# Kernel optimization log

Measured on AMD Instinct MI355X. Metric: run time of the kernel, lower is better.

The kernel has to match this reference:

```python
import jax, jax.numpy as jnp
import numpy as np

B, S, D, H = 2, 2048, 768, 12
E = D // H  # d_head = 64


def setup_inputs() -> dict:
    key = jax.random.key(0)
    ks = jax.random.split(key, 10)
    scale = 1.0 / np.sqrt(D)
    x = jax.random.normal(ks[0], (B, S, D), dtype=jnp.float32)
    # Additive mask, laid out [H*B, S, S] as the torch forward slices per head.
    attn_mask = jnp.zeros((H * B, S, S), dtype=jnp.float32)
    # Per-head projections (math form: q = x @ Wq[h] + bq[h])
    Wq = jax.random.normal(ks[1], (H, D, E), dtype=jnp.float32) * scale
    bq = jax.random.normal(ks[2], (H, E), dtype=jnp.float32) * 0.01
    Wk = jax.random.normal(ks[3], (H, D, E), dtype=jnp.float32) * scale
    bk = jax.random.normal(ks[4], (H, E), dtype=jnp.float32) * 0.01
    Wv = jax.random.normal(ks[5], (H, D, E), dtype=jnp.float32) * scale
    bv = jax.random.normal(ks[6], (H, E), dtype=jnp.float32) * 0.01
    Wo = jax.random.normal(ks[7], (D, D), dtype=jnp.float32) * scale
    bo = jax.random.normal(ks[8], (D,), dtype=jnp.float32) * 0.01
    return {"x": x, "attn_mask": attn_mask, "Wq": Wq, "bq": bq,
            "Wk": Wk, "bk": bk, "Wv": Wv, "bv": bv, "Wo": Wo, "bo": bo}


def reference(x, attn_mask, Wq, bq, Wk, bk, Wv, bv, Wo, bo):
    # x: [B,S,D]; attn_mask: [H*B,S,S]
    q = jnp.einsum('bsd,hde->hbse', x, Wq) + bq[:, None, None, :]
    k = jnp.einsum('bsd,hde->hbse', x, Wk) + bk[:, None, None, :]
    v = jnp.einsum('bsd,hde->hbse', x, Wv) + bv[:, None, None, :]
    mask = attn_mask.reshape(H, B, S, S)
    # NOTE: original code has NO 1/sqrt(d_head) scaling — kept faithful.
    logits = jnp.einsum('hbse,hbte->hbst', q, k) + mask
    w = jax.nn.softmax(logits, axis=-1)  # dropout is identity at eval / p=0
    o = jnp.einsum('hbst,hbte->hbse', w, v)  # [H,B,S,E]
    o = jnp.transpose(o, (1, 2, 0, 3)).reshape(B, S, H * E)  # concat heads
    return o @ Wo + bo
```

## Files before the change

kernel.cpp:

```cpp
#include <hip/hip_runtime.h>
#include <hip/hip_bf16.h>
#include <cmath>

constexpr int Bc  = 2;
constexpr int Sc  = 2048;
constexpr int Dc  = 768;
constexpr int Hc  = 12;
constexpr int Ec  = 64;
constexpr int BSc = Bc * Sc;

typedef _Float16 f16;
typedef __attribute__((ext_vector_type(8)))  _Float16 half8;
typedef __attribute__((ext_vector_type(16))) float    floatx16;

typedef __attribute__((address_space(3))) void       lds_void;
typedef __attribute__((address_space(1))) const void glb_cvoid;


__global__ __launch_bounds__(256) void prep_kernel(
    const float* __restrict__ x,
    const float* __restrict__ Wq, const float* __restrict__ Wk, const float* __restrict__ Wv,
    const float* __restrict__ bq, const float* __restrict__ bk, const float* __restrict__ bv,
    const float* __restrict__ Wo,
    f16* __restrict__ x16, f16* __restrict__ Wt16, f16* __restrict__ Wot16,
    float* __restrict__ bias_cat)
{
    __shared__ __align__(16) float Ts[64][65];
    const int t = threadIdx.x;
    int bid = blockIdx.x;

    if (bid < 1536) {
        const size_t base = (size_t)bid * 2048 + t * 8;
        const float4 v0 = *(const float4*)(x + base);
        const float4 v1 = *(const float4*)(x + base + 4);
        half8 hv;
        hv[0] = (f16)v0.x; hv[1] = (f16)v0.y; hv[2] = (f16)v0.z; hv[3] = (f16)v0.w;
        hv[4] = (f16)v1.x; hv[5] = (f16)v1.y; hv[6] = (f16)v1.z; hv[7] = (f16)v1.w;
        *(half8*)(x16 + base) = hv;
        return;
    }
    bid -= 1536;
    if (bid < 432) {
        const int proj = bid / 144, rem = bid % 144, h = rem / 12, dt = rem % 12;
        const float* W = ((proj == 0) ? Wq : (proj == 1) ? Wk : Wv) + (size_t)h * Dc * Ec;
        const int c = t & 63, rr = t >> 6;
        #pragma unroll
        for (int r0 = 0; r0 < 64; r0 += 4) {
            const int d = rr + r0;
            Ts[d][c] = W[(size_t)(dt * 64 + d) * Ec + c];
        }
        __syncthreads();
        #pragma unroll
        for (int r0 = 0; r0 < 64; r0 += 4) {
            const int e = rr + r0;
            Wt16[(size_t)(proj * 768 + h * 64 + e) * Dc + dt * 64 + c] = (f16)Ts[c][e];
        }
        return;
    }
    bid -= 432;
    if (bid < 144) {
        const int rt = bid / 12, ct = bid % 12;
        const int c = t & 63, rr = t >> 6;
        #pragma unroll
        for (int r0 = 0; r0 < 64; r0 += 4) {
            const int d = rr + r0;
            Ts[d][c] = Wo[(size_t)(rt * 64 + d) * Dc + ct * 64 + c];
        }
        __syncthreads();
        #pragma unroll
        for (int r0 = 0; r0 < 64; r0 += 4) {
            const int e = rr + r0;
            Wot16[(size_t)(ct * 64 + e) * Dc + rt * 64 + c] = (f16)Ts[c][e];
        }
        return;
    }
    bid -= 144;
    {
        const int g = bid * 256 + t;
        if (g < 3 * 768) {
            const int proj = g / 768, idx = g % 768;
            const float* bb = (proj == 0) ? bq : (proj == 1) ? bk : bv;
            bias_cat[g] = bb[idx];
        }
    }
}

__global__ __launch_bounds__(256, 2) void gemm_qkv_kernel(
    const f16* __restrict__ x16, const f16* __restrict__ Wt16,
    const float* __restrict__ bias_cat,
    f16* __restrict__ q16, f16* __restrict__ kswz, f16* __restrict__ vswz)
{
    __shared__ __align__(16) unsigned char smem[34816];
    f16 (*As)[64]  = (f16(*)[64])smem;
    f16 (*Bs)[64]  = (f16(*)[64])(smem + 16384);
    f16 (*Cs)[136] = (f16(*)[136])smem;

    const int t = threadIdx.x;
    const int wave = t >> 6, lane = t & 63;
    const int col = lane & 31, hf = lane >> 5;
    const int wr = wave & 1, wc = wave >> 1;
    const int m0 = blockIdx.x * 128, n0 = blockIdx.y * 128;
    const int lrow = lane >> 3, lseg = lane & 7;
    const int sseg = lseg ^ lrow;
    const int sw   = (col & 7) << 3;

    floatx16 c00, c01, c10, c11;
    #pragma unroll
    for (int i = 0; i < 16; ++i) { c00[i] = 0.f; c01[i] = 0.f; c10[i] = 0.f; c11[i] = 0.f; }

    for (int k0 = 0; k0 < Dc; k0 += 64) {
        #pragma unroll
        for (int i = 0; i < 4; ++i) {
            const int r = wave * 32 + i * 8;
            __builtin_amdgcn_global_load_lds(
                (glb_cvoid*)(x16 + (size_t)(m0 + r + lrow) * Dc + k0 + sseg * 8),
                (lds_void*)&As[r][0], 16, 0, 0);
            __builtin_amdgcn_global_load_lds(
                (glb_cvoid*)(Wt16 + (size_t)(n0 + r + lrow) * Dc + k0 + sseg * 8),
                (lds_void*)&Bs[r][0], 16, 0, 0);
        }
        __syncthreads();
        #pragma unroll
        for (int ks = 0; ks < 4; ++ks) {
            const int fo = (ks * 16 + hf * 8) ^ sw;
            const half8 a0 = *(const half8*)&As[wr * 64 + col][fo];
            const half8 a1 = *(const half8*)&As[wr * 64 + 32 + col][fo];
            const half8 b0 = *(const half8*)&Bs[wc * 64 + col][fo];
            const half8 b1 = *(const half8*)&Bs[wc * 64 + 32 + col][fo];
            c00 = __builtin_amdgcn_mfma_f32_32x32x16_f16(a0, b0, c00, 0, 0, 0);
            c01 = __builtin_amdgcn_mfma_f32_32x32x16_f16(a0, b1, c01, 0, 0, 0);
            c10 = __builtin_amdgcn_mfma_f32_32x32x16_f16(a1, b0, c10, 0, 0, 0);
            c11 = __builtin_amdgcn_mfma_f32_32x32x16_f16(a1, b1, c11, 0, 0, 0);
        }
        __syncthreads();
    }

    const float bias0 = bias_cat[n0 + wc * 64 + col];
    const float bias1 = bias_cat[n0 + wc * 64 + 32 + col];
    #pragma unroll
    for (int i = 0; i < 16; ++i) {
        const int r = (i & 3) + 8 * (i >> 2) + 4 * hf;
        Cs[wr * 64 + r][wc * 64 + col]           = (f16)(c00[i] + bias0);
        Cs[wr * 64 + r][wc * 64 + 32 + col]      = (f16)(c01[i] + bias1);
        Cs[wr * 64 + 32 + r][wc * 64 + col]      = (f16)(c10[i] + bias0);
        Cs[wr * 64 + 32 + r][wc * 64 + 32 + col] = (f16)(c11[i] + bias1);
    }
    __syncthreads();

    const int proj = n0 / 768;
    const int h0   = (n0 - proj * 768) >> 6;
    const int b    = m0 >> 11;
    const int s_in = m0 & 2047;
    const int kt0  = s_in >> 5;

    if (proj == 0) {
        const int row = t >> 1, seg = t & 1;
        const int h = h0 + seg;
        f16* gp = q16 + ((size_t)(h * Bc + b) * Sc + s_in + row) * Ec;
        #pragma unroll
        for (int j = 0; j < 8; ++j)
            *(half8*)(gp + j * 8) = *(const half8*)&Cs[row][seg * 64 + j * 8];
    } else if (proj == 1) {
        #pragma unroll
        for (int ch = 0; ch < 8; ++ch) {
            const int id = ch * 256 + t;
            const int lane_ = id & 63;
            const int ks  = (id >> 6) & 3;
            const int ktp = (id >> 8) & 3;
            const int seg = (id >> 10) & 1;
            const int colp = lane_ & 31, hfp = lane_ >> 5;
            const int hb = (h0 + seg) * Bc + b;
            const half8 val = *(const half8*)&Cs[ktp * 32 + colp][seg * 64 + ks * 16 + hfp * 8];
            *(half8*)(kswz + ((size_t)((hb * 64 + kt0 + ktp) * 4 + ks) << 9) + lane_ * 8) = val;
        }
    } else {
        #pragma unroll
        for (int ch = 0; ch < 8; ++ch) {
            const int id = ch * 256 + t;
            const int lane_ = id & 63;
            const int ks2 = (id >> 6) & 1;
            const int vh  = (id >> 7) & 1;
            const int ktp = (id >> 8) & 3;
            const int seg = (id >> 10) & 1;
            const int colp = lane_ & 31, hfp = lane_ >> 5;
            const int hb = (h0 + seg) * Bc + b;
            const int e  = vh * 32 + colp;
            half8 val;
            #pragma unroll
            for (int j = 0; j < 8; ++j)
                val[j] = Cs[ktp * 32 + ks2 * 16 + hfp * 8 + j][seg * 64 + e];
            *(half8*)(vswz + ((size_t)(((hb * 64 + kt0 + ktp) * 2 + ks2) * 2 + vh) << 9) + lane_ * 8) = val;
        }
    }
}

__global__ __launch_bounds__(128, 2) void flash_attn_kernel(
    const f16* __restrict__ q16, const f16* __restrict__ kswz,
    const f16* __restrict__ vswz, const float* __restrict__ mask,
    f16* __restrict__ obuf16)
{
    __shared__ _Float16 Plds[2][32][44];

    const int fblk = blockIdx.x;
    const int kk   = fblk >> 3;
    const int hb   = (fblk & 7) + 8 * (kk >> 5);
    const int rb   = kk & 31;
    const int h    = hb >> 1;
    const int b    = hb & 1;

    const int t    = threadIdx.x;
    const int wave = t >> 6;
    const int lane = t & 63;
    const int col  = lane & 31;
    const int hf   = lane >> 5;
    const int row0 = rb * 64 + wave * 32;

    const f16* qb  = q16  + ((size_t)hb * Sc + row0) * Ec;
    const f16* kbz = kswz + ((size_t)hb << 17);
    const f16* vbz = vswz + ((size_t)hb << 17);
    const float* mband = mask + ((size_t)hb * Sc + rb * 64) * Sc;

    half8 qfrag[4];
    #pragma unroll
    for (int ks = 0; ks < 4; ++ks)
        qfrag[ks] = *(const half8*)(qb + (size_t)col * Ec + ks * 16 + hf * 8);

    constexpr int NT = Sc / 32;

    float vmax[16];
    #pragma unroll
    for (int i = 0; i < 16; ++i) vmax[i] = -3e38f;

    half8 kreg[4];
    {
        const f16* kp = kbz + lane * 8;
        #pragma unroll
        for (int ks = 0; ks < 4; ++ks) kreg[ks] = *(const half8*)(kp + (ks << 9));
    }
    #pragma unroll 2
    for (int kt = 0; kt < NT; ++kt) {
        floatx16 c;
        #pragma unroll
        for (int i = 0; i < 16; ++i) c[i] = 0.f;
        #pragma unroll
        for (int ks = 0; ks < 4; ++ks)
            c = __builtin_amdgcn_mfma_f32_32x32x16_f16(qfrag[ks], kreg[ks], c, 0, 0, 0);
        if (kt + 1 < NT) {
            const f16* kp = kbz + ((size_t)(kt + 1) << 11) + lane * 8;
            #pragma unroll
            for (int ks = 0; ks < 4; ++ks) kreg[ks] = *(const half8*)(kp + (ks << 9));
        }
        #pragma unroll
        for (int i = 0; i < 16; ++i) vmax[i] = fmaxf(vmax[i], c[i]);
    }
    float mrow[16];
    #pragma unroll
    for (int i = 0; i < 16; ++i) {
        float v = vmax[i];
        v = fmaxf(v, __shfl_xor(v, 1));
        v = fmaxf(v, __shfl_xor(v, 2));
        v = fmaxf(v, __shfl_xor(v, 4));
        v = fmaxf(v, __shfl_xor(v, 8));
        v = fmaxf(v, __shfl_xor(v, 16));
        mrow[i] = v;
    }

    floatx16 o0, o1;
    float lsum[16];
    #pragma unroll
    for (int i = 0; i < 16; ++i) { o0[i] = 0.f; o1[i] = 0.f; lsum[i] = 0.f; }

    const float* mlane = mband + (size_t)(wave * 32 + 4 * hf) * Sc + col;

    float ma[16], mb[16];
    #pragma unroll
    for (int i = 0; i < 16; ++i)
        ma[i] = __builtin_nontemporal_load(
            mlane + (size_t)((i & 3) + 8 * (i >> 2)) * Sc);

    {
        const f16* kp = kbz + lane * 8;
        #pragma unroll
        for (int ks = 0; ks < 4; ++ks) kreg[ks] = *(const half8*)(kp + (ks << 9));
    }

#define ATT_TILE(KT, MC, MN)                                                   \
    do {                                                                       \
        const int kt_ = (KT);                                                  \
        const f16* vp_ = vbz + ((size_t)kt_ << 11) + lane * 8;                 \
        const half8 va_ = *(const half8*)(vp_);                                \
        const half8 vb_ = *(const half8*)(vp_ + (1 << 9));                     \
        const half8 vc_ = *(const half8*)(vp_ + (2 << 9));                     \
        const half8 vd_ = *(const half8*)(vp_ + (3 << 9));                     \
        if (kt_ + 1 < NT) {                                                    \
            const float* mp_ = mlane + (kt_ + 1) * 32;                         \
            _Pragma("unroll")                                                  \
            for (int i = 0; i < 16; ++i)                                       \
                MN[i] = __builtin_nontemporal_load(                            \
                    mp_ + (size_t)((i & 3) + 8 * (i >> 2)) * Sc);              \
        }                                                                      \
        floatx16 c_;                                                           \
        _Pragma("unroll")                                                      \
        for (int i = 0; i < 16; ++i) c_[i] = 0.f;                              \
        _Pragma("unroll")                                                      \
        for (int ks = 0; ks < 4; ++ks)                                         \
            c_ = __builtin_amdgcn_mfma_f32_32x32x16_f16(qfrag[ks], kreg[ks],   \
                                                        c_, 0, 0, 0);          \
        if (kt_ + 1 < NT) {                                                    \
            const f16* kp_ = kbz + ((size_t)(kt_ + 1) << 11) + lane * 8;       \
            _Pragma("unroll")                                                  \
            for (int ks = 0; ks < 4; ++ks)                                     \
                kreg[ks] = *(const half8*)(kp_ + (ks << 9));                   \
        }                                                                      \
        _Pragma("unroll")                                                      \
        for (int i = 0; i < 16; ++i) {                                         \
            const int r_ = (i & 3) + 8 * (i >> 2) + 4 * hf;                    \
            const float p_ = __expf(c_[i] + MC[i] - mrow[i]);         \
            lsum[i] += p_;                                                     \
            Plds[wave][r_][col] = (f16)p_;                                     \
        }                                                                      \
                       \
        asm volatile("s_waitcnt lgkmcnt(0)" ::: "memory");                     \
        _Pragma("unroll")                                                      \
        for (int ks2 = 0; ks2 < 2; ++ks2) {                                    \
            const half8 pf_ = *(const half8*)(&Plds[wave][col][ks2 * 16 + hf * 8]); \
            o0 = __builtin_amdgcn_mfma_f32_32x32x16_f16(                       \
                pf_, (ks2 == 0) ? va_ : vc_, o0, 0, 0, 0);                     \
            o1 = __builtin_amdgcn_mfma_f32_32x32x16_f16(                       \
                pf_, (ks2 == 0) ? vb_ : vd_, o1, 0, 0, 0);                     \
        }                                                                      \
    } while (0)

    for (int kt2 = 0; kt2 < NT; kt2 += 2) {
        ATT_TILE(kt2,     ma, mb);
        ATT_TILE(kt2 + 1, mb, ma);
    }
#undef ATT_TILE

    #pragma unroll
    for (int i = 0; i < 16; ++i) {
        float v = lsum[i];
        v += __shfl_xor(v, 1);
        v += __shfl_xor(v, 2);
        v += __shfl_xor(v, 4);
        v += __shfl_xor(v, 8);
        v += __shfl_xor(v, 16);
        const float inv = 1.f / v;
        const int r = (i & 3) + 8 * (i >> 2) + 4 * hf;
        const size_t orow = ((size_t)b * Sc + row0 + r) * Dc + h * Ec;
        obuf16[orow + col]      = (f16)(o0[i] * inv);
        obuf16[orow + 32 + col] = (f16)(o1[i] * inv);
    }
}

__global__ __launch_bounds__(256, 2) void gemm_out_kernel(
    const f16* __restrict__ a16, const f16* __restrict__ Wot16,
    const float* __restrict__ bo, float* __restrict__ out)
{
    __shared__ __align__(16) f16 As[128][64];
    __shared__ __align__(16) f16 Bs[64][64];

    const int t = threadIdx.x;
    const int wave = t >> 6, lane = t & 63;
    const int col = lane & 31, hf = lane >> 5;
    const int m0 = blockIdx.x * 128, n0 = blockIdx.y * 64;
    const int lrow = lane >> 3, lseg = lane & 7;
    const int sseg = lseg ^ lrow;
    const int sw   = (col & 7) << 3;

    floatx16 c0, c1;
    #pragma unroll
    for (int i = 0; i < 16; ++i) { c0[i] = 0.f; c1[i] = 0.f; }

    for (int k0 = 0; k0 < Dc; k0 += 64) {
        #pragma unroll
        for (int i = 0; i < 4; ++i) {
            const int r = wave * 32 + i * 8;
            __builtin_amdgcn_global_load_lds(
                (glb_cvoid*)(a16 + (size_t)(m0 + r + lrow) * Dc + k0 + sseg * 8),
                (lds_void*)&As[r][0], 16, 0, 0);
        }
        {
            const int r = wave * 16;
            __builtin_amdgcn_global_load_lds(
                (glb_cvoid*)(Wot16 + (size_t)(n0 + r + lrow) * Dc + k0 + sseg * 8),
                (lds_void*)&Bs[r][0], 16, 0, 0);
            __builtin_amdgcn_global_load_lds(
                (glb_cvoid*)(Wot16 + (size_t)(n0 + r + 8 + lrow) * Dc + k0 + sseg * 8),
                (lds_void*)&Bs[r + 8][0], 16, 0, 0);
        }
        __syncthreads();
        #pragma unroll
        for (int ks = 0; ks < 4; ++ks) {
            const int fo = (ks * 16 + hf * 8) ^ sw;
            const half8 a  = *(const half8*)&As[wave * 32 + col][fo];
            const half8 b0 = *(const half8*)&Bs[col][fo];
            const half8 b1 = *(const half8*)&Bs[32 + col][fo];
            c0 = __builtin_amdgcn_mfma_f32_32x32x16_f16(a, b0, c0, 0, 0, 0);
            c1 = __builtin_amdgcn_mfma_f32_32x32x16_f16(a, b1, c1, 0, 0, 0);
        }
        __syncthreads();
    }

    const float bo0 = bo[n0 + col], bo1 = bo[n0 + 32 + col];
    #pragma unroll
    for (int i = 0; i < 16; ++i) {
        const int r = (i & 3) + 8 * (i >> 2) + 4 * hf;
        const size_t ro = (size_t)(m0 + wave * 32 + r) * Dc + n0;
        out[ro + col]      = c0[i] + bo0;
        out[ro + 32 + col] = c1[i] + bo1;
    }
}

extern "C" void kernel_launch(void* const* d_in, const int* in_sizes, int n_in,
                              void* d_out, int out_size, void* d_ws, size_t ws_size,
                              hipStream_t stream)
{
    const float* x    = (const float*)d_in[0];
    const float* mask = (const float*)d_in[1];
    const float* Wq   = (const float*)d_in[2];
    const float* bq   = (const float*)d_in[3];
    const float* Wk   = (const float*)d_in[4];
    const float* bk   = (const float*)d_in[5];
    const float* Wv   = (const float*)d_in[6];
    const float* bv   = (const float*)d_in[7];
    const float* Wo   = (const float*)d_in[8];
    const float* bo   = (const float*)d_in[9];
    float* out = (float*)d_out;

    constexpr size_t NQ = (size_t)Hc * Bc * Sc * Ec;
    f16* x16    = (f16*)d_ws;
    f16* Wt16   = x16 + (size_t)BSc * Dc;
    f16* Wot16  = Wt16 + (size_t)3 * Dc * Dc;
    f16* q16    = Wot16 + (size_t)Dc * Dc;
    f16* kswz   = q16 + NQ;
    f16* vswz   = kswz + NQ;
    f16* obuf16 = vswz + NQ;
    float* bias_cat = (float*)(obuf16 + NQ);

    prep_kernel<<<2121, 256, 0, stream>>>(x, Wq, Wk, Wv, bq, bk, bv, Wo,
                                          x16, Wt16, Wot16, bias_cat);

    gemm_qkv_kernel<<<dim3(BSc / 128, 2304 / 128), 256, 0, stream>>>(
        x16, Wt16, bias_cat, q16, kswz, vswz);

    flash_attn_kernel<<<768, 128, 0, stream>>>(
        q16, kswz, vswz, mask, obuf16);

    gemm_out_kernel<<<dim3(BSc / 128, Dc / 64), 256, 0, stream>>>(
        obuf16, Wot16, bo, out);
}
```

Before: 619.2 us.

## Double-buffer LDS tiles in GEMMs and deepen mask prefetch in attention

Both projection GEMMs now use two LDS buffers. The next K-tile is loaded with global_load_lds while the current tile feeds the MFMAs, which removes one barrier per iteration and hides load latency. The attention kernel prefetches mask tiles two steps ahead using four register arrays instead of two. The cost is more LDS per block (64KB for the QKV GEMM), which may reduce occupancy, and more registers in attention, which may cause spills.

```diff
diff --git a/kernel.cpp b/kernel.cpp
--- a/kernel.cpp
+++ b/kernel.cpp
@@ -90,9 +90,7 @@
     const float* __restrict__ bias_cat,
     f16* __restrict__ q16, f16* __restrict__ kswz, f16* __restrict__ vswz)
 {
-    __shared__ __align__(16) unsigned char smem[34816];
-    f16 (*As)[64]  = (f16(*)[64])smem;
-    f16 (*Bs)[64]  = (f16(*)[64])(smem + 16384);
+    __shared__ __align__(16) unsigned char smem[65536];
     f16 (*Cs)[136] = (f16(*)[136])smem;
 
     const int t = threadIdx.x;
@@ -108,18 +106,28 @@
     #pragma unroll
     for (int i = 0; i < 16; ++i) { c00[i] = 0.f; c01[i] = 0.f; c10[i] = 0.f; c11[i] = 0.f; }
 
-    for (int k0 = 0; k0 < Dc; k0 += 64) {
-        #pragma unroll
-        for (int i = 0; i < 4; ++i) {
-            const int r = wave * 32 + i * 8;
-            __builtin_amdgcn_global_load_lds(
-                (glb_cvoid*)(x16 + (size_t)(m0 + r + lrow) * Dc + k0 + sseg * 8),
-                (lds_void*)&As[r][0], 16, 0, 0);
-            __builtin_amdgcn_global_load_lds(
-                (glb_cvoid*)(Wt16 + (size_t)(n0 + r + lrow) * Dc + k0 + sseg * 8),
-                (lds_void*)&Bs[r][0], 16, 0, 0);
-        }
-        __syncthreads();
+#define QKV_STAGE(BUF, K0)                                                     \
+    do {                                                                       \
+        f16 (*As_)[64] = (f16(*)[64])(smem + (BUF) * 32768);                   \
+        f16 (*Bs_)[64] = (f16(*)[64])(smem + (BUF) * 32768 + 16384);           \
+        _Pragma("unroll")                                                      \
+        for (int i_ = 0; i_ < 4; ++i_) {                                       \
+            const int r_ = wave * 32 + i_ * 8;                                 \
+            __builtin_amdgcn_global_load_lds(                                  \
+                (glb_cvoid*)(x16 + (size_t)(m0 + r_ + lrow) * Dc + (K0) + sseg * 8), \
+                (lds_void*)&As_[r_][0], 16, 0, 0);                             \
+            __builtin_amdgcn_global_load_lds(                                  \
+                (glb_cvoid*)(Wt16 + (size_t)(n0 + r_ + lrow) * Dc + (K0) + sseg * 8), \
+                (lds_void*)&Bs_[r_][0], 16, 0, 0);                             \
+        }                                                                      \
+    } while (0)
+
+    QKV_STAGE(0, 0);
+    __syncthreads();
+    for (int tt = 0; tt < 12; ++tt) {
+        if (tt + 1 < 12) QKV_STAGE((tt + 1) & 1, (tt + 1) * 64);
+        f16 (*As)[64] = (f16(*)[64])(smem + (tt & 1) * 32768);
+        f16 (*Bs)[64] = (f16(*)[64])(smem + (tt & 1) * 32768 + 16384);
         #pragma unroll
         for (int ks = 0; ks < 4; ++ks) {
             const int fo = (ks * 16 + hf * 8) ^ sw;
@@ -134,6 +142,7 @@
         }
         __syncthreads();
     }
+#undef QKV_STAGE
 
     const float bias0 = bias_cat[n0 + wc * 64 + col];
     const float bias1 = bias_cat[n0 + wc * 64 + 32 + col];
@@ -272,11 +281,15 @@
 
     const float* mlane = mband + (size_t)(wave * 32 + 4 * hf) * Sc + col;
 
-    float ma[16], mb[16];
+    float m0r[16], m1r[16], m2r[16], m3r[16];
     #pragma unroll
     for (int i = 0; i < 16; ++i)
-        ma[i] = __builtin_nontemporal_load(
+        m0r[i] = __builtin_nontemporal_load(
             mlane + (size_t)((i & 3) + 8 * (i >> 2)) * Sc);
+    #pragma unroll
+    for (int i = 0; i < 16; ++i)
+        m1r[i] = __builtin_nontemporal_load(
+            mlane + 32 + (size_t)((i & 3) + 8 * (i >> 2)) * Sc);
 
     {
         const f16* kp = kbz + lane * 8;
@@ -292,8 +305,8 @@
         const half8 vb_ = *(const half8*)(vp_ + (1 << 9));                     \
         const half8 vc_ = *(const half8*)(vp_ + (2 << 9));                     \
         const half8 vd_ = *(const half8*)(vp_ + (3 << 9));                     \
-        if (kt_ + 1 < NT) {                                                    \
-            const float* mp_ = mlane + (kt_ + 1) * 32;                         \
+        if (kt_ + 2 < NT) {                                                    \
+            const float* mp_ = mlane + (kt_ + 2) * 32;                         \
             _Pragma("unroll")                                                  \
             for (int i = 0; i < 16; ++i)                                       \
                 MN[i] = __builtin_nontemporal_load(                            \
@@ -331,9 +344,11 @@
         }                                                                      \
     } while (0)
 
-    for (int kt2 = 0; kt2 < NT; kt2 += 2) {
-        ATT_TILE(kt2,     ma, mb);
-        ATT_TILE(kt2 + 1, mb, ma);
+    for (int kt4 = 0; kt4 < NT; kt4 += 4) {
+        ATT_TILE(kt4,     m0r, m2r);
+        ATT_TILE(kt4 + 1, m1r, m3r);
+        ATT_TILE(kt4 + 2, m2r, m0r);
+        ATT_TILE(kt4 + 3, m3r, m1r);
     }
 #undef ATT_TILE
 
@@ -357,8 +372,7 @@
     const f16* __restrict__ a16, const f16* __restrict__ Wot16,
     const float* __restrict__ bo, float* __restrict__ out)
 {
-    __shared__ __align__(16) f16 As[128][64];
-    __shared__ __align__(16) f16 Bs[64][64];
+    __shared__ __align__(16) unsigned char smem[49152];
 
     const int t = threadIdx.x;
     const int wave = t >> 6, lane = t & 63;
@@ -372,24 +386,34 @@
     #pragma unroll
     for (int i = 0; i < 16; ++i) { c0[i] = 0.f; c1[i] = 0.f; }
 
-    for (int k0 = 0; k0 < Dc; k0 += 64) {
-        #pragma unroll
-        for (int i = 0; i < 4; ++i) {
-            const int r = wave * 32 + i * 8;
-            __builtin_amdgcn_global_load_lds(
-                (glb_cvoid*)(a16 + (size_t)(m0 + r + lrow) * Dc + k0 + sseg * 8),
-                (lds_void*)&As[r][0], 16, 0, 0);
-        }
-        {
-            const int r = wave * 16;
-            __builtin_amdgcn_global_load_lds(
-                (glb_cvoid*)(Wot16 + (size_t)(n0 + r + lrow) * Dc + k0 + sseg * 8),
-                (lds_void*)&Bs[r][0], 16, 0, 0);
-            __builtin_amdgcn_global_load_lds(
-                (glb_cvoid*)(Wot16 + (size_t)(n0 + r + 8 + lrow) * Dc + k0 + sseg * 8),
-                (lds_void*)&Bs[r + 8][0], 16, 0, 0);
-        }
-        __syncthreads();
+#define OUT_STAGE(BUF, K0)                                                     \
+    do {                                                                       \
+        f16 (*As_)[64] = (f16(*)[64])(smem + (BUF) * 24576);                   \
+        f16 (*Bs_)[64] = (f16(*)[64])(smem + (BUF) * 24576 + 16384);           \
+        _Pragma("unroll")                                                      \
+        for (int i_ = 0; i_ < 4; ++i_) {                                       \
+            const int r_ = wave * 32 + i_ * 8;                                 \
+            __builtin_amdgcn_global_load_lds(                                  \
+                (glb_cvoid*)(a16 + (size_t)(m0 + r_ + lrow) * Dc + (K0) + sseg * 8), \
+                (lds_void*)&As_[r_][0], 16, 0, 0);                             \
+        }                                                                      \
+        {                                                                      \
+            const int r_ = wave * 16;                                          \
+            __builtin_amdgcn_global_load_lds(                                  \
+                (glb_cvoid*)(Wot16 + (size_t)(n0 + r_ + lrow) * Dc + (K0) + sseg * 8), \
+                (lds_void*)&Bs_[r_][0], 16, 0, 0);                             \
+            __builtin_amdgcn_global_load_lds(                                  \
+                (glb_cvoid*)(Wot16 + (size_t)(n0 + r_ + 8 + lrow) * Dc + (K0) + sseg * 8), \
+                (lds_void*)&Bs_[r_ + 8][0], 16, 0, 0);                         \
+        }                                                                      \
+    } while (0)
+
+    OUT_STAGE(0, 0);
+    __syncthreads();
+    for (int tt = 0; tt < 12; ++tt) {
+        if (tt + 1 < 12) OUT_STAGE((tt + 1) & 1, (tt + 1) * 64);
+        f16 (*As)[64] = (f16(*)[64])(smem + (tt & 1) * 24576);
+        f16 (*Bs)[64] = (f16(*)[64])(smem + (tt & 1) * 24576 + 16384);
         #pragma unroll
         for (int ks = 0; ks < 4; ++ks) {
             const int fo = (ks * 16 + hf * 8) ^ sw;
@@ -401,6 +425,7 @@
         }
         __syncthreads();
     }
+#undef OUT_STAGE
 
     const float bo0 = bo[n0 + col], bo1 = bo[n0 + 32 + col];
     #pragma unroll
```

New measurement: 631.5 us. No clear change (+2.0%).
